# Performance work log

Hardware: AMD Instinct MI355X
Metric: run time of the kernel (lower is better)

## Reference

```python
import jax, jax.numpy as jnp
import numpy as np

N = 50000   # nodes per side
H = 256     # hidden_dim
E = 800000  # edges per metapath (avg degree 16)
XAVIER_STD = 0.088  # gain 1.414 * sqrt(2/(H+H))


def setup_inputs() -> dict:
    key = jax.random.key(0)
    ks = jax.random.split(key, 32)
    inp = {}
    inp["h_d"] = jax.random.normal(ks[0], (N, H), dtype=jnp.float32)
    inp["h_p"] = jax.random.normal(ks[1], (N, H), dtype=jnp.float32)
    i = 2
    for name in ["d0", "d1", "p0", "p1"]:
        inp[name + "_idx"] = jax.random.randint(ks[i], (2, E), 0, N, dtype=jnp.int32); i += 1
        inp[name + "_val"] = jax.random.uniform(ks[i], (E,), dtype=jnp.float32); i += 1
    # per-metapath GCN params: Linear weight [H,H] (no bias), additive bias [H], PReLU slope (scalar)
    for name in ["d0", "d1", "p0", "p1"]:
        inp["W" + name] = jax.random.normal(ks[i], (H, H), dtype=jnp.float32) * XAVIER_STD; i += 1
        inp["b" + name] = jnp.zeros((H,), jnp.float32)
        inp["a" + name] = jnp.full((1,), 0.25, jnp.float32)
    # per-side attention params: fc weight/bias, att vector [1,H]
    for s in ["d", "p"]:
        inp["fcW" + s] = jax.random.normal(ks[i], (H, H), dtype=jnp.float32) * XAVIER_STD; i += 1
        inp["fcb" + s] = jnp.zeros((H,), jnp.float32)
        inp["att" + s] = jax.random.normal(ks[i], (1, H), dtype=jnp.float32) * XAVIER_STD; i += 1
    return inp


def _gcn(h, W, b, a, idx, val):
    # Linear (no bias) -> sparse COO spmm -> bias -> PReLU
    fts = h @ W.T                                  # [N,H]
    msg = val[:, None] * fts[idx[1]]               # gather source rows [E,H]
    out = jax.ops.segment_sum(msg, idx[0], num_segments=h.shape[0]) + b
    return jnp.where(out > 0, out, a * out)        # PReLU, shared slope


def _attn_fuse(embeds, Wf, bf, att):
    # score_p = att . mean_n(tanh(fc(embed_p)))  -> softmax over metapaths
    sp = jnp.stack([jnp.tanh(e @ Wf.T + bf).mean(axis=0) for e in embeds])  # [P,H]
    beta = jax.nn.softmax(sp @ att[0])                                      # [P]
    return jnp.einsum('p,pnh->nh', beta, jnp.stack(embeds))


def reference(h_d, h_p, d0_idx, d0_val, d1_idx, d1_val, p0_idx, p0_val,
              p1_idx, p1_val, Wd0, bd0, ad0, Wd1, bd1, ad1,
              Wp0, bp0, ap0, Wp1, bp1, ap1,
              fcWd, fcbd, attd, fcWp, fcbp, attp):
    embeds_d = [_gcn(h_d, Wd0, bd0, ad0, d0_idx, d0_val),
                _gcn(h_d, Wd1, bd1, ad1, d1_idx, d1_val)]
    z_d = _attn_fuse(embeds_d, fcWd, fcbd, attd)
    embeds_p = [_gcn(h_p, Wp0, bp0, ap0, p0_idx, p0_val),
                _gcn(h_p, Wp1, bp1, ap1, p1_idx, p1_val)]
    z_p = _attn_fuse(embeds_p, fcWp, fcbp, attp)
    return (z_d, z_p)
```

## Files before the change

### kernel.cpp

```cpp
#include <hip/hip_runtime.h>
#include <cstdint>

#define H 256
#define NBMAX 400
#define CAPB 16

typedef unsigned short u16;
typedef __attribute__((ext_vector_type(8))) short short8;
typedef __attribute__((ext_vector_type(4))) float f32x4;

__device__ __forceinline__ float bf2f(u16 u) {
  return __uint_as_float(((unsigned)u) << 16);
}
__device__ __forceinline__ u16 f2bf(float f) {
  unsigned u = __float_as_uint(f);
  u = (u + 0x7FFF + ((u >> 16) & 1)) >> 16;
  return (u16)u;
}
__device__ __forceinline__ void async16(const void* g, void* l) {
  __builtin_amdgcn_global_load_lds((const __attribute__((address_space(1))) void*)g,
                                   (__attribute__((address_space(3))) void*)l, 16, 0, 0);
}

__global__ __launch_bounds__(256) void cvt_bf16(
    const float* __restrict__ h0, const float* __restrict__ h1,
    u16* __restrict__ dst, int total, size_t NH)
{
  const float* src = blockIdx.y ? h1 : h0;
  u16* d = dst + (size_t)blockIdx.y * NH;
  int i = (blockIdx.x * 256 + threadIdx.x) * 4;
  if (i >= total) return;
  float4 x = *(const float4*)(src + i);
  *(ushort4*)(d + i) = make_ushort4(f2bf(x.x), f2bf(x.y), f2bf(x.z), f2bf(x.w));
}

__global__ __launch_bounds__(256) void cvt_weights(
    const float* w0, const float* w1, const float* w2, const float* w3,
    const float* w4, const float* w5, u16* __restrict__ dst)
{
  const float* srcs[6] = {w0, w1, w2, w3, w4, w5};
  const float* s = srcs[blockIdx.y];
  int i = (blockIdx.x * 256 + threadIdx.x) * 4;
  float4 x = *(const float4*)(s + i);
  *(ushort4*)(dst + blockIdx.y * (H * H) + i) =
      make_ushort4(f2bf(x.x), f2bf(x.y), f2bf(x.z), f2bf(x.w));
}

__device__ __forceinline__ int block_incl_scan(int v) {
  __shared__ int wsum[4];
  int tid = threadIdx.x, lane = tid & 63, w = tid >> 6;
  int x = v;
  #pragma unroll
  for (int off = 1; off < 64; off <<= 1) {
    int n = __shfl_up(x, off);
    if (lane >= off) x += n;
  }
  if (lane == 63) wsum[w] = x;
  __syncthreads();
  int add = 0;
  #pragma unroll
  for (int i = 0; i < 4; ++i) add += (i < w) ? wsum[i] : 0;
  return x + add;
}

__global__ __launch_bounds__(1024) void hist_coarse(
    const int* i0, const int* i1, const int* i2, const int* i3,
    int* __restrict__ bcnt, int E, int nbuck)
{
  int mp = blockIdx.y;
  const int* idxs[4] = {i0, i1, i2, i3};
  const int* idx = idxs[mp];
  __shared__ int lh[NBMAX];
  int t = threadIdx.x;
  for (int i = t; i < nbuck; i += 1024) lh[i] = 0;
  __syncthreads();
  for (int e = blockIdx.x * 1024 + t; e < E; e += gridDim.x * 1024)
    atomicAdd(&lh[idx[e] >> 7], 1);
  __syncthreads();
  for (int i = t; i < nbuck; i += 1024) {
    int v = lh[i];
    if (v) atomicAdd(&bcnt[mp * nbuck + i], v);
  }
}

__global__ __launch_bounds__(256) void scan_buckets(
    const int* __restrict__ bcnt, int* __restrict__ bbase,
    int* __restrict__ gcur, int* __restrict__ rowptr, int N, int E, int nbuck)
{
  int mp = blockIdx.y;
  int t = threadIdx.x;
  int i0 = t * 2, i1 = t * 2 + 1;
  int a = (i0 < nbuck) ? bcnt[mp * nbuck + i0] : 0;
  int b = (i1 < nbuck) ? bcnt[mp * nbuck + i1] : 0;
  int s = a + b;
  int incl = block_incl_scan(s);
  int ex = incl - s;
  if (i0 < nbuck) { bbase[mp * nbuck + i0] = ex;     gcur[mp * nbuck + i0] = ex; }
  if (i1 < nbuck) { bbase[mp * nbuck + i1] = ex + a; gcur[mp * nbuck + i1] = ex + a; }
  if (t == 0) rowptr[mp * (N + 1) + N] = E;
}

__global__ __launch_bounds__(1024) void scatter_binned(
    const int* i0, const int* i1, const int* i2, const int* i3,
    const float* v0, const float* v1, const float* v2, const float* v3,
    int* __restrict__ gcur, int2* __restrict__ edgesB, int E, int nbuck)
{
  int mp = blockIdx.y;
  const int* idxs[4] = {i0, i1, i2, i3};
  const float* vals[4] = {v0, v1, v2, v3};
  const int* idx = idxs[mp];
  const float* val = vals[mp];
  int* cur = gcur + mp * nbuck;
  int2* out = edgesB + (size_t)mp * E;

  __shared__ int cnt[NBMAX];
  __shared__ int2 slab[NBMAX * CAPB];
  int t = threadIdx.x;
  for (int i = t; i < nbuck; i += 1024) cnt[i] = 0;
  __syncthreads();

  for (int base_e = blockIdx.x * 2048; base_e < E; base_e += gridDim.x * 2048) {
    #pragma unroll
    for (int u = 0; u < 2; ++u) {
      int e = base_e + u * 1024 + t;
      if (e < E) {
        int d = idx[e];
        int s = idx[E + e];
        float v = val[e];
        int bb = d >> 7;
        int2 pk = make_int2(s | ((d & 127) << 16), __float_as_int(v));
        int slot = atomicAdd(&cnt[bb], 1);
        if (slot < CAPB) slab[bb * CAPB + slot] = pk;
        else {
          int pos = atomicAdd(&cur[bb], 1);
          out[pos] = pk;
        }
      }
    }
    __syncthreads();
    for (int bb = t; bb < nbuck; bb += 1024) {
      int c = cnt[bb];
      if (c > CAPB) c = CAPB;
      if (c >= 8) {
        int ng = c >> 3;
        int pos = atomicAdd(&cur[bb], ng * 8);
        for (int k = 0; k < ng * 8; ++k) out[pos + k] = slab[bb * CAPB + k];
        int r = c & 7;
        for (int k = 0; k < r; ++k)
          slab[bb * CAPB + k] = slab[bb * CAPB + ng * 8 + k];
        cnt[bb] = r;
      }
    }
    __syncthreads();
  }
  for (int bb = t; bb < nbuck; bb += 1024) {
    int c = cnt[bb];
    if (c > CAPB) c = CAPB;
    if (c > 0) {
      int pos = atomicAdd(&cur[bb], c);
      for (int k = 0; k < c; ++k) out[pos + k] = slab[bb * CAPB + k];
    }
  }
}

__global__ __launch_bounds__(256) void bucket_to_csr(
    const int2* __restrict__ edgesB, const int* __restrict__ bbase,
    int* __restrict__ rowptr, int2* __restrict__ edges, int N, int E, int nbuck)
{
  int mp = blockIdx.y;
  int b = blockIdx.x;
  int base = bbase[mp * nbuck + b];
  int endp = (b + 1 < nbuck) ? bbase[mp * nbuck + b + 1] : E;
  int cntE = endp - base;
  const int2* in = edgesB + (size_t)mp * E + base;
  int2* out = edges + (size_t)mp * E;

  __shared__ int h[128], csum[128];
  int t = threadIdx.x;
  if (t < 128) h[t] = 0;
  __syncthreads();
  for (int k = t; k < cntE; k += 256)
    atomicAdd(&h[(in[k].x >> 16) & 127], 1);
  __syncthreads();
  if (t == 0) {
    int acc = 0;
    for (int i = 0; i < 128; ++i) { int c = h[i]; csum[i] = acc; acc += c; }
  }
  __syncthreads();
  int d0 = b << 7;
  if (t < 128 && d0 + t < N) rowptr[mp * (N + 1) + d0 + t] = base + csum[t];
  if (t < 128) h[t] = csum[t];
  __syncthreads();
  for (int k = t; k < cntE; k += 256) {
    int2 pk = in[k];
    int dl = (pk.x >> 16) & 127;
    int pos = atomicAdd(&h[dl], 1);
    out[base + pos] = make_int2(pk.x & 0xFFFF, pk.y);
  }
}

__global__ __launch_bounds__(256) void spmm_csr(
    const u16* __restrict__ ftsAll, const int* __restrict__ rowptrAll,
    const int2* __restrict__ edgesAll,
    const float* b0, const float* b1, const float* b2, const float* b3,
    const float* a0ptr, const float* a1ptr, const float* a2ptr, const float* a3ptr,
    u16* __restrict__ eAll, int N, int E, size_t NH)
{
  int mp = blockIdx.y;
  const u16* fts = ftsAll + (size_t)mp * NH;
  const int* rowptr = rowptrAll + (size_t)mp * (N + 1);
  const int2* edges = edgesAll + (size_t)mp * E;
  const float* biases[4] = {b0, b1, b2, b3};
  const float* alphas[4] = {a0ptr, a1ptr, a2ptr, a3ptr};
  const float* bias = biases[mp];
  const float* alpha = alphas[mp];
  u16* e = eAll + (size_t)mp * NH;

  int gw = (int)((blockIdx.x * 256 + threadIdx.x) >> 6);
  if (gw >= N) return;
  int lane = threadIdx.x & 63;
  int beg = rowptr[gw], end = rowptr[gw + 1];
  float a0 = 0.f, a1 = 0.f, a2 = 0.f, a3 = 0.f;
  for (int base = beg; base < end; base += 64) {
    int k = base + lane;
    int2 ev = make_int2(0, 0);
    if (k < end) ev = edges[k];
    int cnt = min(64, end - base);
    int j = 0;
    for (; j + 4 <= cnt; j += 4) {
      int sj[4]; float vj[4]; ushort4 r[4];
      #pragma unroll
      for (int u = 0; u < 4; ++u) {
        sj[u] = __shfl(ev.x, j + u);
        vj[u] = __uint_as_float((unsigned)__shfl(ev.y, j + u));
      }
      #pragma unroll
      for (int u = 0; u < 4; ++u)
        r[u] = *(const ushort4*)(fts + (size_t)sj[u] * H + lane * 4);
      #pragma unroll
      for (int u = 0; u < 4; ++u) {
        a0 += vj[u] * bf2f(r[u].x);
        a1 += vj[u] * bf2f(r[u].y);
        a2 += vj[u] * bf2f(r[u].z);
        a3 += vj[u] * bf2f(r[u].w);
      }
    }
    for (; j < cnt; ++j) {
      int sj = __shfl(ev.x, j);
      float vj = __uint_as_float((unsigned)__shfl(ev.y, j));
      ushort4 r = *(const ushort4*)(fts + (size_t)sj * H + lane * 4);
      a0 += vj * bf2f(r.x);
      a1 += vj * bf2f(r.y);
      a2 += vj * bf2f(r.z);
      a3 += vj * bf2f(r.w);
    }
  }
  int c = lane * 4;
  float al = alpha[0];
  float r0 = a0 + bias[c],     r1 = a1 + bias[c + 1];
  float r2 = a2 + bias[c + 2], r3 = a3 + bias[c + 3];
  r0 = r0 > 0.f ? r0 : al * r0;
  r1 = r1 > 0.f ? r1 : al * r1;
  r2 = r2 > 0.f ? r2 : al * r2;
  r3 = r3 > 0.f ? r3 : al * r3;
  *(ushort4*)(e + (size_t)gw * H + c) =
      make_ushort4(f2bf(r0), f2bf(r1), f2bf(r2), f2bf(r3));
}

template <int MODE>
__global__ __launch_bounds__(256) void gemm_bt(
    const u16* __restrict__ Abase, const u16* __restrict__ Wbase,
    u16* __restrict__ Cbase, const float* fcb0, const float* fcb1,
    float* __restrict__ colsum, int M, size_t NH)
{
  const int pi = blockIdx.z;
  const u16* A; const u16* W; u16* C = nullptr;
  const float* bias = nullptr; float* cs = nullptr;
  if (MODE == 0) {
    A = Abase + (size_t)(pi >> 1) * NH;
    W = Wbase + (size_t)pi * (H * H);
    C = Cbase + (size_t)pi * NH;
  } else {
    A = Abase + (size_t)pi * NH;
    W = Wbase + (size_t)(pi >> 1) * (H * H);
    bias = (pi >> 1) ? fcb1 : fcb0;
    cs = colsum + (size_t)pi * H;
  }

  __shared__ u16 As[128 * 64];
  __shared__ u16 Bs[128 * 64];
  const int tid  = threadIdx.x;
  const int lane = tid & 63;
  const int wave = tid >> 6;
  const int quad = lane >> 4;
  const int l15  = lane & 15;
  const int m0 = blockIdx.x * 128;
  const int n0 = blockIdx.y * 128;
  const int wr = (wave & 1) * 64;
  const int wc = (wave >> 1) * 64;

  f32x4 acc[4][4] = {};

  for (int k0 = 0; k0 < H; k0 += 64) {
    #pragma unroll
    for (int r = 0; r < 4; ++r) {
      int chunk = r * 256 + tid;
      int row = chunk >> 3;
      int col = (chunk & 7) * 8;
      int gm = m0 + row; if (gm >= M) gm = M - 1;
      u16* lbase = As + (r * 256 + wave * 64) * 8;
      async16(A + (size_t)gm * H + k0 + col, lbase);
      u16* lbase2 = Bs + (r * 256 + wave * 64) * 8;
      async16(W + (size_t)(n0 + row) * H + k0 + col, lbase2);
    }
    __syncthreads();
    #pragma unroll
    for (int kk = 0; kk < 64; kk += 32) {
      short8 af[4], bf[4];
      #pragma unroll
      for (int i = 0; i < 4; ++i) {
        af[i] = *(const short8*)(As + (wr + i * 16 + l15) * 64 + kk + quad * 8);
        bf[i] = *(const short8*)(Bs + (wc + i * 16 + l15) * 64 + kk + quad * 8);
      }
      #pragma unroll
      for (int mi = 0; mi < 4; ++mi)
        #pragma unroll
        for (int ni = 0; ni < 4; ++ni)
          acc[mi][ni] = __builtin_amdgcn_mfma_f32_16x16x32_bf16(af[mi], bf[ni], acc[mi][ni], 0, 0, 0);
    }
    __syncthreads();
  }

  if (MODE == 0) {
    #pragma unroll
    for (int mi = 0; mi < 4; ++mi)
      #pragma unroll
      for (int ni = 0; ni < 4; ++ni) {
        int n = n0 + wc + ni * 16 + l15;
        #pragma unroll
        for (int j = 0; j < 4; ++j) {
          int m = m0 + wr + mi * 16 + quad * 4 + j;
          if (m < M) C[(size_t)m * H + n] = f2bf(acc[mi][ni][j]);
        }
      }
  } else {
    #pragma unroll
    for (int ni = 0; ni < 4; ++ni) {
      int n = n0 + wc + ni * 16 + l15;
      float bv = bias[n];
      float s = 0.f;
      #pragma unroll
      for (int mi = 0; mi < 4; ++mi)
        #pragma unroll
        for (int j = 0; j < 4; ++j) {
          int m = m0 + wr + mi * 16 + quad * 4 + j;
          if (m < M) {
            float x = acc[mi][ni][j] + bv;
            s += 1.f - 2.f / (__expf(2.f * x) + 1.f);
          }
        }
      s += __shfl_xor(s, 16);
      s += __shfl_xor(s, 32);
      if (lane < 16) unsafeAtomicAdd(&cs[n], s);
    }
  }
}

__global__ __launch_bounds__(256) void compute_beta(
    const float* __restrict__ sp, const float* attd, const float* attp,
    float invN, float* __restrict__ beta)
{
  __shared__ float red0[4], red1[4];
  int s = blockIdx.y;
  const float* att = s ? attp : attd;
  const float* spb = sp + (size_t)(2 * s) * H;
  int t = threadIdx.x;
  float a = att[t];
  float s0 = spb[t] * invN * a;
  float s1 = spb[H + t] * invN * a;
  #pragma unroll
  for (int off = 32; off > 0; off >>= 1) {
    s0 += __shfl_down(s0, off);
    s1 += __shfl_down(s1, off);
  }
  int lane = t & 63, w = t >> 6;
  if (lane == 0) { red0[w] = s0; red1[w] = s1; }
  __syncthreads();
  if (t == 0) {
    float a0 = red0[0] + red0[1] + red0[2] + red0[3];
    float a1 = red1[0] + red1[1] + red1[2] + red1[3];
    float mx = fmaxf(a0, a1);
    float e0v = __expf(a0 - mx), e1v = __expf(a1 - mx);
    float inv = 1.f / (e0v + e1v);
    beta[2 * s]     = e0v * inv;
    beta[2 * s + 1] = e1v * inv;
  }
}

__global__ __launch_bounds__(256) void fuse_out(
    const u16* __restrict__ eAll, const float* __restrict__ beta,
    float* __restrict__ out, int total, size_t NH)
{
  int s = blockIdx.y;
  const u16* e0 = eAll + (size_t)(2 * s) * NH;
  const u16* e1 = eAll + (size_t)(2 * s + 1) * NH;
  float* o = out + (size_t)s * NH;
  int i = (blockIdx.x * 256 + threadIdx.x) * 4;
  if (i >= total) return;
  float b0 = beta[2 * s], b1 = beta[2 * s + 1];
  ushort4 u0 = *(const ushort4*)(e0 + i);
  ushort4 u1 = *(const ushort4*)(e1 + i);
  float4 ov;
  ov.x = b0 * bf2f(u0.x) + b1 * bf2f(u1.x);
  ov.y = b0 * bf2f(u0.y) + b1 * bf2f(u1.y);
  ov.z = b0 * bf2f(u0.z) + b1 * bf2f(u1.z);
  ov.w = b0 * bf2f(u0.w) + b1 * bf2f(u1.w);
  *(float4*)(o + i) = ov;
}

extern "C" void kernel_launch(void* const* d_in, const int* in_sizes, int n_in,
                              void* d_out, int out_size, void* d_ws, size_t ws_size,
                              hipStream_t stream)
{
  const float* h_in[2] = {(const float*)d_in[0], (const float*)d_in[1]};
  const int N = in_sizes[0] / H;
  const int E = in_sizes[3];
  const int* idx[4]; const float* val[4];
  for (int i = 0; i < 4; ++i) {
    idx[i] = (const int*)d_in[2 + 2 * i];
    val[i] = (const float*)d_in[3 + 2 * i];
  }
  const float *W[4], *bia[4], *alp[4];
  for (int i = 0; i < 4; ++i) {
    W[i]   = (const float*)d_in[10 + 3 * i];
    bia[i] = (const float*)d_in[11 + 3 * i];
    alp[i] = (const float*)d_in[12 + 3 * i];
  }
  const float *fcW[2], *fcb[2], *att[2];
  for (int s = 0; s < 2; ++s) {
    fcW[s] = (const float*)d_in[22 + 3 * s];
    fcb[s] = (const float*)d_in[23 + 3 * s];
    att[s] = (const float*)d_in[24 + 3 * s];
  }

  const size_t NH = (size_t)N * H;
  const int nbuck = (N + 127) >> 7;
  auto align256 = [](size_t x) { return (x + 255) & ~(size_t)255; };
  char* p = (char*)d_ws;
  u16* hbf = (u16*)p;      p += align256((size_t)2 * NH * 2);
  u16* fts = (u16*)p;      p += align256((size_t)4 * NH * 2);
  u16* eAll = (u16*)p;     p += align256((size_t)4 * NH * 2);
  u16* Wbf = (u16*)p;      p += align256((size_t)6 * H * H * 2);
  int* bcnt = (int*)p;     p += align256((size_t)4 * NBMAX * 4);
  int* bbase = (int*)p;    p += align256((size_t)4 * NBMAX * 4);
  int* gcur = (int*)p;     p += align256((size_t)4 * NBMAX * 4);
  int* rowptr = (int*)p;   p += align256((size_t)4 * (N + 1) * 4);
  int2* edges = (int2*)p;  p += align256((size_t)4 * E * 8);
  float* sp = (float*)p;   p += align256((size_t)4 * H * 4);
  float* beta = (float*)p;
  int2* edgesB = (int2*)fts;

  const int gx = (N + 127) / 128;
  const int tot = (int)NH;
  const int el_blocks = (tot / 4 + 255) / 256;
  const int spmm_blocks = (N + 3) / 4;

  dim3 wgrid(H * H / 1024, 6);
  cvt_weights<<<wgrid, 256, 0, stream>>>(W[0], W[1], W[2], W[3], fcW[0], fcW[1], Wbf);

  hipMemsetAsync(bcnt, 0, (size_t)4 * NBMAX * 4, stream);
  hipMemsetAsync(sp, 0, (size_t)4 * H * 4, stream);
  hist_coarse<<<dim3(64, 4), 1024, 0, stream>>>(idx[0], idx[1], idx[2], idx[3],
                                                bcnt, E, nbuck);
  scan_buckets<<<dim3(1, 4), 256, 0, stream>>>(bcnt, bbase, gcur, rowptr, N, E, nbuck);
  scatter_binned<<<dim3(64, 4), 1024, 0, stream>>>(idx[0], idx[1], idx[2], idx[3],
                                                   val[0], val[1], val[2], val[3],
                                                   gcur, edgesB, E, nbuck);
  bucket_to_csr<<<dim3(nbuck, 4), 256, 0, stream>>>(edgesB, bbase, rowptr, edges,
                                                    N, E, nbuck);

  cvt_bf16<<<dim3(el_blocks, 2), 256, 0, stream>>>(h_in[0], h_in[1], hbf, tot, NH);

  gemm_bt<0><<<dim3(gx, 2, 4), 256, 0, stream>>>(hbf, Wbf, fts,
                                                 nullptr, nullptr, nullptr, N, NH);

  spmm_csr<<<dim3(spmm_blocks, 4), 256, 0, stream>>>(
      fts, rowptr, edges,
      bia[0], bia[1], bia[2], bia[3],
      alp[0], alp[1], alp[2], alp[3],
      eAll, N, E, NH);

  gemm_bt<1><<<dim3(gx, 2, 4), 256, 0, stream>>>(eAll, Wbf + (size_t)4 * H * H,
                                                 nullptr, fcb[0], fcb[1], sp, N, NH);

  compute_beta<<<dim3(1, 2), 256, 0, stream>>>(sp, att[0], att[1],
                                               1.0f / (float)N, beta);

  fuse_out<<<dim3(el_blocks, 2), 256, 0, stream>>>(eAll, beta, (float*)d_out, tot, NH);
}
```

Baseline: 689.8 us.

## Aggregate raw features before the linear transform, fusing bias and PReLU into GEMM

Reorders each GCN layer from gather(h@W^T) to (A·h)@W^T, which linearity allows. The SpMM now gathers rows directly from the two shared bf16 input feature matrices instead of four per-metapath transformed matrices, which should give the gathers better cache reuse. Bias and PReLU move into the first GEMM's epilogue. In exchange, the aggregated sums are rounded to bf16 before the matmul, which changes rounding behaviour, and the GEMM now reads four distinct A matrices instead of two.

```diff
diff --git a/kernel.cpp b/kernel.cpp
--- a/kernel.cpp
+++ b/kernel.cpp
@@ -200,21 +200,15 @@
 }
 
 __global__ __launch_bounds__(256) void spmm_csr(
-    const u16* __restrict__ ftsAll, const int* __restrict__ rowptrAll,
-    const int2* __restrict__ edgesAll,
-    const float* b0, const float* b1, const float* b2, const float* b3,
-    const float* a0ptr, const float* a1ptr, const float* a2ptr, const float* a3ptr,
-    u16* __restrict__ eAll, int N, int E, size_t NH)
+    const u16* __restrict__ hbf, const int* __restrict__ rowptrAll,
+    const int2* __restrict__ edgesAll, u16* __restrict__ aggAll,
+    int N, int E, size_t NH)
 {
   int mp = blockIdx.y;
-  const u16* fts = ftsAll + (size_t)mp * NH;
+  const u16* fts = hbf + (size_t)(mp >> 1) * NH;
   const int* rowptr = rowptrAll + (size_t)mp * (N + 1);
   const int2* edges = edgesAll + (size_t)mp * E;
-  const float* biases[4] = {b0, b1, b2, b3};
-  const float* alphas[4] = {a0ptr, a1ptr, a2ptr, a3ptr};
-  const float* bias = biases[mp];
-  const float* alpha = alphas[mp];
-  u16* e = eAll + (size_t)mp * NH;
+  u16* agg = aggAll + (size_t)mp * NH;
 
   int gw = (int)((blockIdx.x * 256 + threadIdx.x) >> 6);
   if (gw >= N) return;
@@ -256,34 +250,35 @@
     }
   }
   int c = lane * 4;
-  float al = alpha[0];
-  float r0 = a0 + bias[c],     r1 = a1 + bias[c + 1];
-  float r2 = a2 + bias[c + 2], r3 = a3 + bias[c + 3];
-  r0 = r0 > 0.f ? r0 : al * r0;
-  r1 = r1 > 0.f ? r1 : al * r1;
-  r2 = r2 > 0.f ? r2 : al * r2;
-  r3 = r3 > 0.f ? r3 : al * r3;
-  *(ushort4*)(e + (size_t)gw * H + c) =
-      make_ushort4(f2bf(r0), f2bf(r1), f2bf(r2), f2bf(r3));
+  *(ushort4*)(agg + (size_t)gw * H + c) =
+      make_ushort4(f2bf(a0), f2bf(a1), f2bf(a2), f2bf(a3));
 }
 
 template <int MODE>
 __global__ __launch_bounds__(256) void gemm_bt(
     const u16* __restrict__ Abase, const u16* __restrict__ Wbase,
-    u16* __restrict__ Cbase, const float* fcb0, const float* fcb1,
+    u16* __restrict__ Cbase,
+    const float* bp0, const float* bp1, const float* bp2, const float* bp3,
+    const float* ap0, const float* ap1, const float* ap2, const float* ap3,
     float* __restrict__ colsum, int M, size_t NH)
 {
   const int pi = blockIdx.z;
-  const u16* A; const u16* W; u16* C = nullptr;
-  const float* bias = nullptr; float* cs = nullptr;
+  const float* bps[4] = {bp0, bp1, bp2, bp3};
+  const float* aps[4] = {ap0, ap1, ap2, ap3};
+  const u16* A = Abase + (size_t)pi * NH;
+  const u16* W;
+  u16* C = nullptr;
+  const float* bias;
+  float* cs = nullptr;
+  float al = 0.f;
   if (MODE == 0) {
-    A = Abase + (size_t)(pi >> 1) * NH;
     W = Wbase + (size_t)pi * (H * H);
     C = Cbase + (size_t)pi * NH;
+    bias = bps[pi];
+    al = aps[pi][0];
   } else {
-    A = Abase + (size_t)pi * NH;
     W = Wbase + (size_t)(pi >> 1) * (H * H);
-    bias = (pi >> 1) ? fcb1 : fcb0;
+    bias = (pi >> 1) ? bp1 : bp0;
     cs = colsum + (size_t)pi * H;
   }
 
@@ -337,10 +332,15 @@
       #pragma unroll
       for (int ni = 0; ni < 4; ++ni) {
         int n = n0 + wc + ni * 16 + l15;
+        float bv = bias[n];
         #pragma unroll
         for (int j = 0; j < 4; ++j) {
           int m = m0 + wr + mi * 16 + quad * 4 + j;
-          if (m < M) C[(size_t)m * H + n] = f2bf(acc[mi][ni][j]);
+          if (m < M) {
+            float x = acc[mi][ni][j] + bv;
+            x = x > 0.f ? x : al * x;
+            C[(size_t)m * H + n] = f2bf(x);
+          }
         }
       }
   } else {
@@ -448,7 +448,7 @@
   auto align256 = [](size_t x) { return (x + 255) & ~(size_t)255; };
   char* p = (char*)d_ws;
   u16* hbf = (u16*)p;      p += align256((size_t)2 * NH * 2);
-  u16* fts = (u16*)p;      p += align256((size_t)4 * NH * 2);
+  u16* aggAll = (u16*)p;   p += align256((size_t)4 * NH * 2);
   u16* eAll = (u16*)p;     p += align256((size_t)4 * NH * 2);
   u16* Wbf = (u16*)p;      p += align256((size_t)6 * H * H * 2);
   int* bcnt = (int*)p;     p += align256((size_t)4 * NBMAX * 4);
@@ -458,7 +458,7 @@
   int2* edges = (int2*)p;  p += align256((size_t)4 * E * 8);
   float* sp = (float*)p;   p += align256((size_t)4 * H * 4);
   float* beta = (float*)p;
-  int2* edgesB = (int2*)fts;
+  int2* edgesB = (int2*)aggAll;
 
   const int gx = (N + 127) / 128;
   const int tot = (int)NH;
@@ -481,17 +481,20 @@
 
   cvt_bf16<<<dim3(el_blocks, 2), 256, 0, stream>>>(h_in[0], h_in[1], hbf, tot, NH);
 
-  gemm_bt<0><<<dim3(gx, 2, 4), 256, 0, stream>>>(hbf, Wbf, fts,
-                                                 nullptr, nullptr, nullptr, N, NH);
-
   spmm_csr<<<dim3(spmm_blocks, 4), 256, 0, stream>>>(
-      fts, rowptr, edges,
+      hbf, rowptr, edges, aggAll, N, E, NH);
+
+  gemm_bt<0><<<dim3(gx, 2, 4), 256, 0, stream>>>(
+      aggAll, Wbf, eAll,
       bia[0], bia[1], bia[2], bia[3],
       alp[0], alp[1], alp[2], alp[3],
-      eAll, N, E, NH);
-
-  gemm_bt<1><<<dim3(gx, 2, 4), 256, 0, stream>>>(eAll, Wbf + (size_t)4 * H * H,
-                                                 nullptr, fcb[0], fcb[1], sp, N, NH);
+      nullptr, N, NH);
+
+  gemm_bt<1><<<dim3(gx, 2, 4), 256, 0, stream>>>(
+      eAll, Wbf + (size_t)4 * H * H, nullptr,
+      fcb[0], fcb[1], nullptr, nullptr,
+      nullptr, nullptr, nullptr, nullptr,
+      sp, N, NH);
 
   compute_beta<<<dim3(1, 2), 256, 0, stream>>>(sp, att[0], att[1],
                                                1.0f / (float)N, beta);
```

After: 722.4 us. +4.7%, slower.
